# Optimization experiments

Measured on AMD Instinct MI355X. Metric: run time of the kernel, lower is better.

The kernel has to match this reference:

```python
import jax, jax.numpy as jnp
import numpy as np

N_NODES = 100000
N_EDGES = 1_600_000
N_ROIS = 400
HIDDEN = 128
N_GRAPHS = 512
OUT = 2


def setup_inputs() -> dict:
    key = jax.random.key(0)
    ks = jax.random.split(key, 7)
    x = jax.random.normal(ks[0], (N_NODES, N_ROIS), dtype=jnp.float32)
    edge_index = jax.random.randint(ks[1], (2, N_EDGES), 0, N_NODES, dtype=jnp.int32)
    # sorted graph-assignment vector; prepend arange so every graph id is non-empty
    rnd = jax.random.randint(ks[2], (N_NODES - N_GRAPHS,), 0, N_GRAPHS, dtype=jnp.int32)
    batch = jnp.sort(jnp.concatenate([jnp.arange(N_GRAPHS, dtype=jnp.int32), rnd]))
    W = jax.random.normal(ks[3], (N_ROIS, HIDDEN), dtype=jnp.float32) / np.float32(np.sqrt(N_ROIS))
    b = jnp.zeros((HIDDEN,), dtype=jnp.float32)
    lin_W = jax.random.normal(ks[4], (HIDDEN, OUT), dtype=jnp.float32) / np.float32(np.sqrt(HIDDEN))
    lin_b = jnp.zeros((OUT,), dtype=jnp.float32)
    return {"x": x, "edge_index": edge_index, "batch": batch,
            "W": W, "b": b, "lin_W": lin_W, "lin_b": lin_b}


def reference(x, edge_index, batch, W, b, lin_W, lin_b):
    N = x.shape[0]
    # GCNConv: add self-loops, symmetric normalization D^-1/2 (A+I) D^-1/2
    loops = jnp.arange(N, dtype=edge_index.dtype)
    row = jnp.concatenate([edge_index[0], loops])  # source
    col = jnp.concatenate([edge_index[1], loops])  # target
    deg = jax.ops.segment_sum(jnp.ones_like(col, dtype=x.dtype), col, num_segments=N)
    dinv = jnp.where(deg > 0, jax.lax.rsqrt(deg), 0.0)
    norm = dinv[row] * dinv[col]                   # [E+N]
    h = x @ W                                      # [N, H] transform before propagate
    msg = h[row] * norm[:, None]                   # [E+N, H]
    agg = jax.ops.segment_sum(msg, col, num_segments=N) + b
    act = jax.nn.relu(agg)                         # [N, H]
    # global max pool over graph ids (all segments guaranteed non-empty)
    pooled = jax.ops.segment_max(act, batch, num_segments=N_GRAPHS)  # [G, H]
    logits = pooled @ lin_W + lin_b                # [G, OUT]
    return logits, pooled
```

## Files before the change

### kernel.cpp

```cpp
#include <hip/hip_runtime.h>
#include <hip/hip_bf16.h>

#define N_NODES 100000
#define N_EDGES 1600000
#define N_ROIS  400
#define HID     128
#define N_GRAPHS 512
#define NOUT    2
#define NBUCK   391
#define BCAP    8192
#define ECH     4096
#define NPW     16
#define NBLK_BUCKET 391
#define NBLK_PREP   208
#define NBLK_GEMM   782

typedef __attribute__((ext_vector_type(8))) short short8;
typedef __attribute__((ext_vector_type(4))) float f32x4;

static __device__ __forceinline__ unsigned short f2bf(float f) {
  __hip_bfloat16 h = __float2bfloat16(f);
  unsigned short u;
  __builtin_memcpy(&u, &h, 2);
  return u;
}
static __device__ __forceinline__ float bf2f(unsigned short h) {
  return __uint_as_float(((unsigned)h) << 16);
}

static __device__ __forceinline__ void gload_lds16(const unsigned short* g, short* l) {
  __builtin_amdgcn_global_load_lds(
      (const __attribute__((address_space(1))) void*)g,
      (__attribute__((address_space(3))) void*)l, 16, 0, 0);
}

__global__ __launch_bounds__(256) void prep_bucket_k(
    const int* __restrict__ row, const int* __restrict__ col,
    int* __restrict__ bcnt, unsigned int* __restrict__ pairs,
    const float* __restrict__ W, unsigned short* __restrict__ Wf,
    float* __restrict__ pooled0) {
  __shared__ int hist[NBUCK];
  __shared__ int lbase[NBUCK];
  __shared__ int adj[NBUCK];
  __shared__ unsigned int spk[ECH];
  __shared__ unsigned short sbk[ECH];
  __shared__ int sc[256];
  int t = threadIdx.x;
  if (blockIdx.x >= NBLK_BUCKET) {
    int idx = (blockIdx.x - NBLK_BUCKET) * 256 + t;
    if (idx < 13 * 8 * 64 * 8) {
      int u    = idx & 7;
      int lane = (idx >> 3) & 63;
      int nt   = (idx >> 9) & 7;
      int kk5  = idx >> 12;
      int n = nt * 16 + (lane & 15);
      int k = kk5 * 32 + (lane >> 4) * 8 + u;
      Wf[idx] = (k < N_ROIS) ? f2bf(W[k * HID + n]) : (unsigned short)0;
    }
    int z = idx * 2;
    if (z < N_GRAPHS * HID) {
      float2 zz = {0.f, 0.f};
      *(float2*)(pooled0 + z) = zz;
    }
    return;
  }
  for (int b = t; b < NBUCK; b += 256) hist[b] = 0;
  __syncthreads();
  int e0 = blockIdx.x * ECH;
  int mtot = min(ECH, N_EDGES - e0);
  unsigned int pk[16];
  int bk[16], rk[16];
#pragma unroll
  for (int i = 0; i < 16; ++i) {
    int e = e0 + t + i * 256;
    if (e < N_EDGES) {
      int r = row[e], c = col[e];
      bk[i] = c >> 8;
      pk[i] = ((unsigned)r << 8) | (unsigned)(c & 255);
      rk[i] = atomicAdd(&hist[bk[i]], 1);
    } else bk[i] = -1;
  }
  __syncthreads();
  int v0 = hist[t];
  sc[t] = v0;
  __syncthreads();
  for (int off = 1; off < 256; off <<= 1) {
    int v = (t >= off) ? sc[t - off] : 0;
    __syncthreads();
    sc[t] += v;
    __syncthreads();
  }
  lbase[t] = sc[t] - v0;
  int tot0 = sc[255];
  __syncthreads();
  int v1 = (t < NBUCK - 256) ? hist[256 + t] : 0;
  sc[t] = v1;
  __syncthreads();
  for (int off = 1; off < 256; off <<= 1) {
    int v = (t >= off) ? sc[t - off] : 0;
    __syncthreads();
    sc[t] += v;
    __syncthreads();
  }
  if (t < NBUCK - 256) lbase[256 + t] = tot0 + sc[t] - v1;
  __syncthreads();
#pragma unroll
  for (int i = 0; i < 16; ++i)
    if (bk[i] >= 0) {
      int pos = lbase[bk[i]] + rk[i];
      spk[pos] = pk[i];
      sbk[pos] = (unsigned short)bk[i];
    }
  for (int b = t; b < NBUCK; b += 256)
    adj[b] = (hist[b] > 0) ? atomicAdd(&bcnt[b], hist[b]) : 0;
  __syncthreads();
  for (int j = t; j < mtot; j += 256) {
    int b = sbk[j];
    int p = adj[b] + (j - lbase[b]);
    if (p < BCAP) pairs[(size_t)b * BCAP + p] = spk[j];
  }
}

__global__ __launch_bounds__(512, 8) void csr_gemm_k(
    const unsigned int* __restrict__ pairs, const int* __restrict__ bcnt,
    int* __restrict__ csr_row, int* __restrict__ offs, int* __restrict__ cnt,
    float* __restrict__ dinv,
    const float* __restrict__ x, const unsigned short* __restrict__ Wf,
    unsigned short* __restrict__ hp) {
  __shared__ __align__(16) union {
    struct {
      unsigned int ep[BCAP];
      int h[256]; int sc2[256]; int cur[256];
    } c;
    short Bs[16384];
  } u;
  int t = threadIdx.x;

  if (blockIdx.x < NBUCK) {
    bool act = t < 256;
    int b = blockIdx.x;
    int m = min(bcnt[b], BCAP);
    size_t base = (size_t)b * BCAP;
    for (int j = t; j < m; j += 512) u.c.ep[j] = pairs[base + j];
    if (act) u.c.h[t] = 0;
    __syncthreads();
    for (int j = t; j < m; j += 512) atomicAdd(&u.c.h[u.c.ep[j] & 255u], 1);
    __syncthreads();
    int myc = act ? u.c.h[t] : 0;
    int mycp = (myc + 3) & ~3;
    if (act) u.c.sc2[t] = mycp;
    __syncthreads();
    for (int off = 1; off < 256; off <<= 1) {
      int v = (act && t >= off) ? u.c.sc2[t - off] : 0;
      __syncthreads();
      if (act) u.c.sc2[t] += v;
      __syncthreads();
    }
    if (act) {
      int loff = u.c.sc2[t] - mycp;
      u.c.cur[t] = loff;
      int node = b * 256 + t;
      if (node < N_NODES) {
        cnt[node] = myc;
        offs[node] = (int)base + loff;
        dinv[node] = rsqrtf((float)(myc + 1));
      }
    }
    __syncthreads();
    for (int j = t; j < m; j += 512) {
      unsigned int e = u.c.ep[j];
      int pos = atomicAdd(&u.c.cur[e & 255u], 1);
      if (pos < BCAP) csr_row[base + pos] = (int)(e >> 8);
    }
    return;
  }

  int lane = t & 63, wv = t >> 6;
  int mrow = lane & 15, kg = lane >> 4;
  int row0 = (blockIdx.x - NBUCK) * 128;
  int arow = row0 + wv * 16 + mrow;
  bool rowok = arow < N_NODES;
  const float* xp = x + (size_t)arow * N_ROIS;

  f32x4 acc[8];
#pragma unroll
  for (int i = 0; i < 8; ++i) acc[i] = (f32x4){0.f, 0.f, 0.f, 0.f};

  const int pk0[4] = {0, 4, 7, 10};
  const int pnk[4] = {4, 3, 3, 3};

#pragma unroll
  for (int ph = 0; ph < 4; ++ph) {
    int cbase = pk0[ph] * 8;
#pragma unroll
    for (int c = 0; c < pnk[ph]; ++c) {
      int ch = wv * pnk[ph] + c;
      gload_lds16(Wf + ((size_t)cbase + ch) * 512 + lane * 8, &u.Bs[ch * 512]);
    }
    asm volatile("s_waitcnt vmcnt(0)" ::: "memory");
    __syncthreads();
#pragma unroll
    for (int kfl = 0; kfl < pnk[ph]; ++kfl) {
      int kf = pk0[ph] + kfl;
      int k0 = kf * 32 + kg * 8;
      short8 a8;
      if (rowok && k0 + 8 <= N_ROIS) {
        float4 f0 = *(const float4*)(xp + k0);
        float4 f1 = *(const float4*)(xp + k0 + 4);
        a8[0] = (short)f2bf(f0.x); a8[1] = (short)f2bf(f0.y);
        a8[2] = (short)f2bf(f0.z); a8[3] = (short)f2bf(f0.w);
        a8[4] = (short)f2bf(f1.x); a8[5] = (short)f2bf(f1.y);
        a8[6] = (short)f2bf(f1.z); a8[7] = (short)f2bf(f1.w);
      } else {
#pragma unroll
        for (int v = 0; v < 8; ++v) {
          int k = k0 + v;
          float f = (rowok && k < N_ROIS) ? xp[k] : 0.f;
          a8[v] = (short)f2bf(f);
        }
      }
#pragma unroll
      for (int nt = 0; nt < 8; ++nt) {
        short8 bf = *(const short8*)&u.Bs[(kfl * 8 + nt) * 512 + lane * 8];
        acc[nt] = __builtin_amdgcn_mfma_f32_16x16x32_bf16(a8, bf, acc[nt], 0, 0, 0);
      }
    }
    __syncthreads();
  }

#pragma unroll
  for (int r = 0; r < 4; ++r) {
    int grow = row0 + wv * 16 + kg * 4 + r;
    if (grow < N_NODES) {
      unsigned short* op = hp + (size_t)grow * HID + mrow;
#pragma unroll
      for (int nt = 0; nt < 8; ++nt) op[nt * 16] = f2bf(acc[nt][r]);
    }
  }
}

static __device__ __forceinline__ void acc8s(float* a, uint4 u, float d) {
  a[0] = fmaf(d, bf2f((unsigned short)(u.x)), a[0]);
  a[1] = fmaf(d, bf2f((unsigned short)(u.x >> 16)), a[1]);
  a[2] = fmaf(d, bf2f((unsigned short)(u.y)), a[2]);
  a[3] = fmaf(d, bf2f((unsigned short)(u.y >> 16)), a[3]);
  a[4] = fmaf(d, bf2f((unsigned short)(u.z)), a[4]);
  a[5] = fmaf(d, bf2f((unsigned short)(u.z >> 16)), a[5]);
  a[6] = fmaf(d, bf2f((unsigned short)(u.w)), a[6]);
  a[7] = fmaf(d, bf2f((unsigned short)(u.w >> 16)), a[7]);
}

__global__ __launch_bounds__(256) void gather_k(
    const unsigned short* __restrict__ hp, const int* __restrict__ csr_row,
    const int* __restrict__ offs, const int* __restrict__ cnt,
    const float* __restrict__ dinv, const int* __restrict__ batch,
    const float* __restrict__ bias, unsigned int* __restrict__ pooled_bits) {
  int wave = (blockIdx.x * blockDim.x + threadIdx.x) >> 6;
  int lane = threadIdx.x & 63;
  int g  = lane >> 4;
  int cg = lane & 15;
  int n0 = wave * NPW;
  if (n0 >= N_NODES) return;
  int nend = min(n0 + NPW, N_NODES);
  float bv[8];
  {
    float4 b0 = *(const float4*)(bias + cg * 8);
    float4 b1 = *(const float4*)(bias + cg * 8 + 4);
    bv[0] = b0.x; bv[1] = b0.y; bv[2] = b0.z; bv[3] = b0.w;
    bv[4] = b1.x; bv[5] = b1.y; bv[6] = b1.z; bv[7] = b1.w;
  }
  float rm[8];
#pragma unroll
  for (int k = 0; k < 8; ++k) rm[k] = 0.f;
  int cur_g = batch[n0];

  for (int i = n0; i < nend; ++i) {
    int start = offs[i];
    int m = cnt[i];
    float di = dinv[i];
    float a[8];
#pragma unroll
    for (int k = 0; k < 8; ++k) a[k] = 0.f;
    if (g == 0) {
      uint4 u = *(const uint4*)(hp + (size_t)i * HID + cg * 8);
      acc8s(a, u, di);
    }
    for (int j = 0; j < m; j += 4) {
      int4 q = *(const int4*)(csr_row + start + j);
      int s = (g == 0) ? q.x : (g == 1) ? q.y : (g == 2) ? q.z : q.w;
      if (j + g < m) {
        float dv = dinv[s];
        uint4 u = *(const uint4*)(hp + (size_t)s * HID + cg * 8);
        acc8s(a, u, dv);
      }
    }
#pragma unroll
    for (int k = 0; k < 8; ++k) {
      a[k] += __shfl_xor(a[k], 16);
      a[k] += __shfl_xor(a[k], 32);
    }
    int gb = batch[i];
    if (gb != cur_g) {
      if (lane < 16) {
#pragma unroll
        for (int k = 0; k < 8; ++k)
          atomicMax(&pooled_bits[cur_g * HID + cg * 8 + k], __float_as_uint(rm[k]));
      }
#pragma unroll
      for (int k = 0; k < 8; ++k) rm[k] = 0.f;
      cur_g = gb;
    }
#pragma unroll
    for (int k = 0; k < 8; ++k)
      rm[k] = fmaxf(rm[k], fmaxf(fmaf(di, a[k], bv[k]), 0.f));
  }
  if (lane < 16) {
#pragma unroll
    for (int k = 0; k < 8; ++k)
      atomicMax(&pooled_bits[cur_g * HID + cg * 8 + k], __float_as_uint(rm[k]));
  }
}

__global__ void logits_k(const float* __restrict__ pooled, const float* __restrict__ lin_W,
                         const float* __restrict__ lin_b, float* __restrict__ out) {
  int t = blockIdx.x * blockDim.x + threadIdx.x;
  if (t < N_GRAPHS * NOUT) {
    int g = t >> 1, o = t & 1;
    float s = lin_b[o];
    const float* pg = pooled + g * HID;
#pragma unroll 8
    for (int k = 0; k < HID; ++k) s = fmaf(pg[k], lin_W[k * NOUT + o], s);
    out[t] = s;
  }
}

extern "C" void kernel_launch(void* const* d_in, const int* in_sizes, int n_in,
                              void* d_out, int out_size, void* d_ws, size_t ws_size,
                              hipStream_t stream) {
  (void)in_sizes; (void)n_in; (void)ws_size; (void)out_size;
  const float* x     = (const float*)d_in[0];
  const int*   ei    = (const int*)d_in[1];
  const int*   row   = ei;
  const int*   col   = ei + N_EDGES;
  const int*   batch = (const int*)d_in[2];
  const float* W     = (const float*)d_in[3];
  const float* b     = (const float*)d_in[4];
  const float* lin_W = (const float*)d_in[5];
  const float* lin_b = (const float*)d_in[6];
  float* out = (float*)d_out;
  float* pooled0 = out + N_GRAPHS * NOUT;

  char* ws = (char*)d_ws;
  int*   bcnt    = (int*)(ws + 0);
  int*   offs    = (int*)(ws + 4096);
  int*   cnt     = (int*)(ws + 404096);
  float* dinv    = (float*)(ws + 804096);
  unsigned short* Wf = (unsigned short*)(ws + 1204096);
  int*   csr_row = (int*)(ws + 1310720);
  unsigned int* pairs = (unsigned int*)(ws + 14123008);
  unsigned short* hp  = (unsigned short*)(ws + 26935296);

  hipMemsetAsync(bcnt, 0, NBUCK * sizeof(int), stream);

  prep_bucket_k<<<NBLK_BUCKET + NBLK_PREP, 256, 0, stream>>>(
      row, col, bcnt, pairs, W, Wf, pooled0);
  csr_gemm_k<<<NBUCK + NBLK_GEMM, 512, 0, stream>>>(
      pairs, bcnt, csr_row, offs, cnt, dinv, x, Wf, hp);
  {
    int waves = (N_NODES + NPW - 1) / NPW;
    int blocks = (waves * 64 + 255) / 256;
    gather_k<<<blocks, 256, 0, stream>>>(
        hp, csr_row, offs, cnt, dinv, batch, b,
        (unsigned int*)pooled0);
  }
  logits_k<<<(N_GRAPHS * NOUT + 255) / 256, 256, 0, stream>>>(
      pooled0, lin_W, lin_b, out);
}
```

Measured before the change: 390.0 us.

## Pre-convert x to padded bf16 buffer and preload all A fragments in GEMM

Adds a pass to the prep kernel that converts x from fp32 to bf16 into a workspace buffer with rows padded to 416 entries. The GEMM then loads all 13 A-operand k-fragments into registers up front instead of converting fp32 inline per k-step, and its launch bound drops from 8 to 4 blocks per SM to make room for those registers. The aim is to remove per-step conversion and tail-guard branches from the MFMA loop and issue all x loads early to hide latency. In exchange, total traffic over x grows: the full fp32 x is still read once, plus a bf16 copy is written and read back, and occupancy may fall.

Measured after the change: 386.4 us. No clear change (-0.9%).

```diff
diff --git a/kernel.cpp b/kernel.cpp
--- a/kernel.cpp
+++ b/kernel.cpp
@@ -13,7 +13,9 @@
 #define NPW     16
 #define NBLK_BUCKET 391
 #define NBLK_PREP   208
+#define NBLK_XCONV  20313
 #define NBLK_GEMM   782
+#define XROW 416
 
 typedef __attribute__((ext_vector_type(8))) short short8;
 typedef __attribute__((ext_vector_type(4))) float f32x4;
@@ -38,6 +40,7 @@
     const int* __restrict__ row, const int* __restrict__ col,
     int* __restrict__ bcnt, unsigned int* __restrict__ pairs,
     const float* __restrict__ W, unsigned short* __restrict__ Wf,
+    const float* __restrict__ x, unsigned short* __restrict__ xb,
     float* __restrict__ pooled0) {
   __shared__ int hist[NBUCK];
   __shared__ int lbase[NBUCK];
@@ -46,6 +49,27 @@
   __shared__ unsigned short sbk[ECH];
   __shared__ int sc[256];
   int t = threadIdx.x;
+  if (blockIdx.x >= NBLK_BUCKET + NBLK_PREP) {
+    int idx = (blockIdx.x - NBLK_BUCKET - NBLK_PREP) * 256 + t;
+    int n = idx / 52, rem = idx - n * 52;
+    if (n < N_NODES) {
+      int k0 = rem * 8;
+      short8 v;
+      if (k0 + 8 <= N_ROIS) {
+        const float* xp = x + (size_t)n * N_ROIS + k0;
+        float4 f0 = *(const float4*)xp;
+        float4 f1 = *(const float4*)(xp + 4);
+        v[0] = (short)f2bf(f0.x); v[1] = (short)f2bf(f0.y);
+        v[2] = (short)f2bf(f0.z); v[3] = (short)f2bf(f0.w);
+        v[4] = (short)f2bf(f1.x); v[5] = (short)f2bf(f1.y);
+        v[6] = (short)f2bf(f1.z); v[7] = (short)f2bf(f1.w);
+      } else {
+        v = (short8){0, 0, 0, 0, 0, 0, 0, 0};
+      }
+      *(short8*)(xb + (size_t)n * XROW + k0) = v;
+    }
+    return;
+  }
   if (blockIdx.x >= NBLK_BUCKET) {
     int idx = (blockIdx.x - NBLK_BUCKET) * 256 + t;
     if (idx < 13 * 8 * 64 * 8) {
@@ -121,11 +145,11 @@
   }
 }
 
-__global__ __launch_bounds__(512, 8) void csr_gemm_k(
+__global__ __launch_bounds__(512, 4) void csr_gemm_k(
     const unsigned int* __restrict__ pairs, const int* __restrict__ bcnt,
     int* __restrict__ csr_row, int* __restrict__ offs, int* __restrict__ cnt,
     float* __restrict__ dinv,
-    const float* __restrict__ x, const unsigned short* __restrict__ Wf,
+    const unsigned short* __restrict__ xb, const unsigned short* __restrict__ Wf,
     unsigned short* __restrict__ hp) {
   __shared__ __align__(16) union {
     struct {
@@ -179,8 +203,12 @@
   int mrow = lane & 15, kg = lane >> 4;
   int row0 = (blockIdx.x - NBUCK) * 128;
   int arow = row0 + wv * 16 + mrow;
-  bool rowok = arow < N_NODES;
-  const float* xp = x + (size_t)arow * N_ROIS;
+  const unsigned short* xr = xb + (size_t)arow * XROW + kg * 8;
+
+  short8 xa[13];
+#pragma unroll
+  for (int kf = 0; kf < 13; ++kf)
+    xa[kf] = *(const short8*)(xr + kf * 32);
 
   f32x4 acc[8];
 #pragma unroll
@@ -202,27 +230,10 @@
 #pragma unroll
     for (int kfl = 0; kfl < pnk[ph]; ++kfl) {
       int kf = pk0[ph] + kfl;
-      int k0 = kf * 32 + kg * 8;
-      short8 a8;
-      if (rowok && k0 + 8 <= N_ROIS) {
-        float4 f0 = *(const float4*)(xp + k0);
-        float4 f1 = *(const float4*)(xp + k0 + 4);
-        a8[0] = (short)f2bf(f0.x); a8[1] = (short)f2bf(f0.y);
-        a8[2] = (short)f2bf(f0.z); a8[3] = (short)f2bf(f0.w);
-        a8[4] = (short)f2bf(f1.x); a8[5] = (short)f2bf(f1.y);
-        a8[6] = (short)f2bf(f1.z); a8[7] = (short)f2bf(f1.w);
-      } else {
-#pragma unroll
-        for (int v = 0; v < 8; ++v) {
-          int k = k0 + v;
-          float f = (rowok && k < N_ROIS) ? xp[k] : 0.f;
-          a8[v] = (short)f2bf(f);
-        }
-      }
 #pragma unroll
       for (int nt = 0; nt < 8; ++nt) {
         short8 bf = *(const short8*)&u.Bs[(kfl * 8 + nt) * 512 + lane * 8];
-        acc[nt] = __builtin_amdgcn_mfma_f32_16x16x32_bf16(a8, bf, acc[nt], 0, 0, 0);
+        acc[nt] = __builtin_amdgcn_mfma_f32_16x16x32_bf16(xa[kf], bf, acc[nt], 0, 0, 0);
       }
     }
     __syncthreads();
@@ -359,13 +370,14 @@
   int*   csr_row = (int*)(ws + 1310720);
   unsigned int* pairs = (unsigned int*)(ws + 14123008);
   unsigned short* hp  = (unsigned short*)(ws + 26935296);
+  unsigned short* xb  = (unsigned short*)(ws + 52535296);
 
   hipMemsetAsync(bcnt, 0, NBUCK * sizeof(int), stream);
 
-  prep_bucket_k<<<NBLK_BUCKET + NBLK_PREP, 256, 0, stream>>>(
-      row, col, bcnt, pairs, W, Wf, pooled0);
+  prep_bucket_k<<<NBLK_BUCKET + NBLK_PREP + NBLK_XCONV, 256, 0, stream>>>(
+      row, col, bcnt, pairs, W, Wf, x, xb, pooled0);
   csr_gemm_k<<<NBUCK + NBLK_GEMM, 512, 0, stream>>>(
-      pairs, bcnt, csr_row, offs, cnt, dinv, x, Wf, hp);
+      pairs, bcnt, csr_row, offs, cnt, dinv, xb, Wf, hp);
   {
     int waves = (N_NODES + NPW - 1) / NPW;
     int blocks = (waves * 64 + 255) / 256;
```
